# Kernel optimization log

Hardware: AMD Instinct MI355X
Metric: run time of the kernel (lower is better)

The kernel has to match this reference:

```python
import jax, jax.numpy as jnp
import numpy as np

GDEP = 3
ALPHA = 0.05
C_IN = 32
C_OUT = 32


def setup_inputs() -> dict:
    key = jax.random.key(0)
    k1, k2, k3, k4 = jax.random.split(key, 4)
    B, C, V, L = 16, C_IN, 512, 168
    x = jax.random.normal(k1, (B, C, V, L), dtype=jnp.float32)
    adj = jax.random.uniform(k2, (V, V), dtype=jnp.float32)
    fan_in = (GDEP + 1) * C_IN  # Conv2d 1x1: kaiming-uniform-ish init
    bound = 1.0 / np.sqrt(fan_in)
    W = jax.random.uniform(k3, (C_OUT, fan_in), minval=-bound, maxval=bound, dtype=jnp.float32)
    b = jax.random.uniform(k4, (C_OUT,), minval=-bound, maxval=bound, dtype=jnp.float32)
    return {"x": x, "adj": adj, "W": W, "b": b}


def reference(x, adj, W, b):
    V = adj.shape[0]
    a = adj + jnp.eye(V, dtype=adj.dtype)
    d = a.sum(axis=1)
    a = a / d[:, None]                      # row-normalized adjacency [V, V]
    h = x
    outs = [h]
    for _ in range(GDEP):                   # small fixed depth loop
        prop = jnp.einsum('ncvl,vw->ncwl', h, a)
        h = ALPHA * x + (1.0 - ALPHA) * prop
        outs.append(h)
    ho = jnp.concatenate(outs, axis=1)      # [B, (gdep+1)*C, V, L]
    # 1x1 conv == channel contraction
    out = jnp.einsum('bcvl,oc->bovl', ho, W) + b[None, :, None, None]
    return out
```

## Files before the change

kernel.cpp:

```cpp
#include <hip/hip_runtime.h>

#define V 512
#define L 168
#define PLANE 86016
#define CHSTRIDE 2752512
#define B_ 16
#define HDRE 1052672

typedef __attribute__((ext_vector_type(8))) short s16x8;
typedef __attribute__((ext_vector_type(4))) float f32x4;
typedef unsigned short u16;

__device__ inline short f2bf(float f) {
    unsigned u = __builtin_bit_cast(unsigned, f);
    u += 0x7FFF + ((u >> 16) & 1);
    return (short)(u >> 16);
}
__device__ inline float bf2f(u16 s) {
    return __builtin_bit_cast(float, ((unsigned)s) << 16);
}
__device__ inline void gll16(const u16* g, u16* lds) {
    __builtin_amdgcn_global_load_lds(
        (const __attribute__((address_space(1))) void*)g,
        (__attribute__((address_space(3))) void*)lds, 16, 0, 0);
}

__global__ __launch_bounds__(256) void prep2(const float* __restrict__ adj,
                                             const float* __restrict__ W,
                                             u16* __restrict__ M1,
                                             u16* __restrict__ ANb,
                                             u16* __restrict__ Wb) {
    if (blockIdx.x == V) {
        const float al = 0.05f, be = 0.95f;
        for (int i = threadIdx.x; i < 1024; i += 256) {
            const int o = i >> 5, c = i & 31;
            const float w0 = W[o * 128 + c];
            const float w1 = W[o * 128 + 32 + c];
            const float w2 = W[o * 128 + 64 + c];
            const float w3 = W[o * 128 + 96 + c];
            Wb[o * 128 + c]      = f2bf(w0 + al * (w1 + w2 + w3));
            Wb[o * 128 + 32 + c] = f2bf(be * (w1 + al * (w2 + w3)));
            Wb[o * 128 + 64 + c] = f2bf(be * be * (w2 + al * w3));
            Wb[o * 128 + 96 + c] = f2bf(be * be * be * w3);
        }
        return;
    }
    const int v = blockIdx.x;
    float s = 0.f;
    for (int w = threadIdx.x; w < V; w += 256)
        s += adj[v * V + w] + (w == v ? 1.f : 0.f);
    __shared__ float red[256];
    red[threadIdx.x] = s;
    __syncthreads();
    for (int off = 128; off > 0; off >>= 1) {
        if ((int)threadIdx.x < off) red[threadIdx.x] += red[threadIdx.x + off];
        __syncthreads();
    }
    const float inv = 1.f / red[0];
    for (int w = threadIdx.x; w < V; w += 256) {
        const short q = f2bf((adj[v * V + w] + (w == v ? 1.f : 0.f)) * inv);
        M1[w * V + v] = q;
        ANb[v * V + w] = q;
    }
}

__global__ __launch_bounds__(256) void powk(const u16* __restrict__ X,
                                            const u16* __restrict__ ANb,
                                            u16* __restrict__ OUT) {
    const int w0 = (blockIdx.x >> 3) * 64, v0 = (blockIdx.x & 7) * 64;
    const int tid = threadIdx.x, lane = tid & 63, wave = tid >> 6;
    const int colb = lane & 15, kg = lane >> 4;
    f32x4 acc[4];
#pragma unroll
    for (int i = 0; i < 4; i++) acc[i] = (f32x4){0.f, 0.f, 0.f, 0.f};
#pragma unroll 4
    for (int kk = 0; kk < 16; kk++) {
        const int u = kk * 32 + kg * 8;
        const s16x8 bfr = *(const s16x8*)&ANb[(size_t)(v0 + wave * 16 + colb) * 512 + u];
#pragma unroll
        for (int mt = 0; mt < 4; mt++) {
            const s16x8 afr = *(const s16x8*)&X[(size_t)(w0 + mt * 16 + colb) * 512 + u];
            acc[mt] = __builtin_amdgcn_mfma_f32_16x16x32_bf16(afr, bfr, acc[mt], 0, 0, 0);
        }
    }
#pragma unroll
    for (int mt = 0; mt < 4; mt++)
#pragma unroll
        for (int r = 0; r < 4; r++)
            OUT[(size_t)(w0 + mt * 16 + kg * 4 + r) * 512 + v0 + wave * 16 + colb] =
                (u16)f2bf(acc[mt][r]);
}

__global__ __launch_bounds__(256) void cvtT(const float* __restrict__ x,
                                            u16* __restrict__ xa) {
    const int b = blockIdx.z >> 5, c = blockIdx.z & 31;
    const int v0 = blockIdx.y * 64, l0 = blockIdx.x * 64;
    const int tid = threadIdx.x;
    __shared__ float T[64][65];
    const float* xp = x + (size_t)b * CHSTRIDE + (size_t)c * PLANE;
    u16* xo = xa + (size_t)b * CHSTRIDE;
#pragma unroll
    for (int rep = 0; rep < 16; rep++) {
        const int idx = rep * 256 + tid;
        const int vv = idx >> 6, ll = idx & 63;
        if (l0 + ll < L) T[vv][ll] = xp[(size_t)(v0 + vv) * L + l0 + ll];
    }
    __syncthreads();
#pragma unroll
    for (int rep = 0; rep < 16; rep++) {
        const int idx = rep * 256 + tid;
        const int ll = idx >> 6, vv = idx & 63;
        if (l0 + ll < L)
            xo[(size_t)((l0 + ll) * 32 + c) * 512 + v0 + vv] = f2bf(T[vv][ll]);
    }
}

__global__ __launch_bounds__(256, 2) void propOut(const u16* __restrict__ xa,
                                                  const u16* __restrict__ AS,
                                                  const u16* __restrict__ Wb,
                                                  const float* __restrict__ bias,
                                                  u16* __restrict__ tmpb) {
    const int b = blockIdx.z;
    const int logical = (blockIdx.x & 7) * 21 + (blockIdx.x >> 3);
    const int ntile = logical >> 2, wq = logical & 3;
    const int n0 = ntile * 128, w0 = wq * 128, l0 = ntile * 4;
    const int tid = threadIdx.x, lane = tid & 63, wave = tid >> 6;
    const int wm = wave >> 1, wn = wave & 1;
    const int colb = lane & 15, kg = lane >> 4;
    __shared__ __align__(16) u16 SH[2][16384];
    u16* flat = &SH[0][0];
    const size_t sB = (size_t)b * CHSTRIDE;
    const u16* srcb = xa + sB;

    const u16* gsrc = (wave == 3) ? srcb + (size_t)n0 * 512
                                  : AS + (size_t)wave * 262144 + (size_t)w0 * 512;

    f32x4 acc1[4][4], acc2[4][4], acc3[4][4];
#pragma unroll
    for (int i = 0; i < 4; i++)
#pragma unroll
        for (int j = 0; j < 4; j++) {
            acc1[i][j] = (f32x4){0.f, 0.f, 0.f, 0.f};
            acc2[i][j] = acc1[i][j];
            acc3[i][j] = acc1[i][j];
        }

#define STAGE(T, BUF)                                                             \
    {                                                                             \
        const int v0s = (T) * 32;                                                 \
        _Pragma("unroll") for (int i = 0; i < 8; i++) {                           \
            const int oct = i >> 1, half = i & 1;                                 \
            const int row = half * 64 + lane;                                     \
            gll16(gsrc + (size_t)row * 512 + v0s + oct * 8,                       \
                  &SH[BUF][wave * 4096 + oct * 1024 + half * 512]);               \
        }                                                                         \
    }

#define MFMASTEP(BUF)                                                             \
    {                                                                             \
        s16x8 bfr[4];                                                             \
        _Pragma("unroll") for (int nt = 0; nt < 4; nt++)                          \
            bfr[nt] = *(const s16x8*)&SH[BUF][12288 + kg * 1024 +                 \
                                             (wn * 64 + nt * 16 + colb) * 8];     \
        _Pragma("unroll") for (int mt = 0; mt < 4; mt++) {                        \
            const int aoff = kg * 1024 + (wm * 64 + mt * 16 + colb) * 8;          \
            const s16x8 a1 = *(const s16x8*)&SH[BUF][aoff];                       \
            const s16x8 a2 = *(const s16x8*)&SH[BUF][4096 + aoff];                \
            const s16x8 a3 = *(const s16x8*)&SH[BUF][8192 + aoff];                \
            _Pragma("unroll") for (int nt = 0; nt < 4; nt++) {                    \
                acc1[mt][nt] = __builtin_amdgcn_mfma_f32_16x16x32_bf16(           \
                    a1, bfr[nt], acc1[mt][nt], 0, 0, 0);                          \
                acc2[mt][nt] = __builtin_amdgcn_mfma_f32_16x16x32_bf16(           \
                    a2, bfr[nt], acc2[mt][nt], 0, 0, 0);                          \
                acc3[mt][nt] = __builtin_amdgcn_mfma_f32_16x16x32_bf16(           \
                    a3, bfr[nt], acc3[mt][nt], 0, 0, 0);                          \
            }                                                                     \
        }                                                                         \
    }

    STAGE(0, 0);
    __syncthreads();
#pragma unroll
    for (int t = 0; t < 16; t++) {
        const int buf = t & 1;
        if (t < 15) STAGE(t + 1, buf ^ 1);
        __builtin_amdgcn_s_setprio(1);
        MFMASTEP(buf);
        __builtin_amdgcn_s_setprio(0);
        __syncthreads();
    }
#undef MFMASTEP
#undef STAGE

#define BOUNCE(ACC)                                                               \
    _Pragma("unroll") for (int mt = 0; mt < 4; mt++) {                            \
        const int wr = wm * 64 + mt * 16 + kg * 4;                                \
        _Pragma("unroll") for (int nt = 0; nt < 4; nt++) {                        \
            const int nn = wn * 64 + nt * 16 + colb;                              \
            _Pragma("unroll") for (int r = 0; r < 4; r++)                         \
                flat[(wr + r) * 136 + nn] = (u16)f2bf(ACC[mt][nt][r]);            \
        }                                                                         \
    }

#define OUTACC(KP)                                                                \
    _Pragma("unroll") for (int pf = 0; pf < 8; pf++) {                            \
        const s16x8 bfr = *(const s16x8*)&flat[(pf * 16 + colb) * 136 +           \
                                               wave * 32 + kg * 8];               \
        _Pragma("unroll") for (int mt = 0; mt < 2; mt++) {                        \
            const s16x8 afr = *(const s16x8*)&Wb[(mt * 16 + colb) * 128 +         \
                                                 (KP) * 32 + kg * 8];             \
            aco[mt][pf] = __builtin_amdgcn_mfma_f32_16x16x32_bf16(                \
                afr, bfr, aco[mt][pf], 0, 0, 0);                                  \
        }                                                                         \
    }

    BOUNCE(acc1);
    __syncthreads();

    f32x4 aco[2][8];
#pragma unroll
    for (int i = 0; i < 2; i++)
#pragma unroll
        for (int j = 0; j < 8; j++) aco[i][j] = (f32x4){0.f, 0.f, 0.f, 0.f};

#pragma unroll
    for (int pf = 0; pf < 8; pf++) {
        s16x8 bfr;
#pragma unroll
        for (int j = 0; j < 8; j++)
            bfr[j] = (short)srcb[(size_t)(n0 + wave * 32 + kg * 8 + j) * 512 +
                                 w0 + pf * 16 + colb];
#pragma unroll
        for (int mt = 0; mt < 2; mt++) {
            const s16x8 afr = *(const s16x8*)&Wb[(mt * 16 + colb) * 128 + kg * 8];
            aco[mt][pf] = __builtin_amdgcn_mfma_f32_16x16x32_bf16(afr, bfr, aco[mt][pf], 0, 0, 0);
        }
    }
    OUTACC(1);
    __syncthreads();
    BOUNCE(acc2);
    __syncthreads();
    OUTACC(2);
    __syncthreads();
    BOUNCE(acc3);
    __syncthreads();
    OUTACC(3);
#undef BOUNCE
#undef OUTACC

#pragma unroll
    for (int mt = 0; mt < 2; mt++)
#pragma unroll
        for (int pf = 0; pf < 8; pf++)
#pragma unroll
            for (int r = 0; r < 4; r++) {
                const int o = mt * 16 + kg * 4 + r;
                tmpb[sB + (size_t)o * PLANE + (size_t)(l0 + wave) * 512 +
                     w0 + pf * 16 + colb] = (u16)f2bf(bias[o] + aco[mt][pf][r]);
            }
}

__global__ __launch_bounds__(256) void transT_b(const u16* __restrict__ tmpb,
                                                float* __restrict__ out) {
    const int o = blockIdx.y, b = blockIdx.z;
    const int vt = blockIdx.x / 3, lt = blockIdx.x % 3;
    const int v0 = vt * 64, l0 = lt * 64;
    const int tid = threadIdx.x;
    __shared__ float T[64][65];
    const u16* tp = tmpb + (size_t)b * CHSTRIDE + (size_t)o * PLANE;
    float* op = out + (size_t)b * CHSTRIDE + (size_t)o * PLANE;
#pragma unroll
    for (int rep = 0; rep < 16; rep++) {
        const int idx = rep * 256 + tid;
        const int ll = idx >> 6, vv = idx & 63;
        if (l0 + ll < L) T[ll][vv] = bf2f(tp[(size_t)(l0 + ll) * 512 + v0 + vv]);
    }
    __syncthreads();
#pragma unroll
    for (int rep = 0; rep < 16; rep++) {
        const int idx = rep * 256 + tid;
        const int vv = idx >> 6, ll = idx & 63;
        if (l0 + ll < L) op[(size_t)(v0 + vv) * L + l0 + ll] = T[ll][vv];
    }
}

extern "C" void kernel_launch(void* const* d_in, const int* in_sizes, int n_in,
                              void* d_out, int out_size, void* d_ws, size_t ws_size,
                              hipStream_t stream) {
    const float* x = (const float*)d_in[0];
    const float* adj = (const float*)d_in[1];
    const float* W = (const float*)d_in[2];
    const float* bias = (const float*)d_in[3];
    float* out = (float*)d_out;

    u16* hdr = (u16*)((char*)d_out + (size_t)out_size * 4 - (size_t)HDRE * 2 - 256);
    u16* AS = hdr;
    u16* M1 = AS;
    u16* M2 = AS + 262144;
    u16* M3 = AS + 2 * 262144;
    u16* ANb = AS + 3 * 262144;
    u16* Wb = AS + 4 * 262144;
    u16* hbuf = (u16*)d_ws;

    prep2<<<V + 1, 256, 0, stream>>>(adj, W, M1, ANb, Wb);
    powk<<<64, 256, 0, stream>>>(M1, ANb, M2);
    powk<<<64, 256, 0, stream>>>(M2, ANb, M3);

    int nbc = (int)(ws_size / ((size_t)4 * CHSTRIDE));
    if (nbc < 1) nbc = 1;
    if (nbc > B_) nbc = B_;

    for (int b0 = 0; b0 < B_; b0 += nbc) {
        const int nb = (B_ - b0 < nbc) ? (B_ - b0) : nbc;
        const float* xb = x + (size_t)b0 * CHSTRIDE;
        float* outb = out + (size_t)b0 * CHSTRIDE;
        u16* xa = hbuf;
        u16* tmpb = hbuf + (size_t)nbc * CHSTRIDE;

        cvtT<<<dim3(3, 8, nb * 32), 256, 0, stream>>>(xb, xa);
        propOut<<<dim3(168, 1, nb), 256, 0, stream>>>(xa, AS, Wb, bias, tmpb);
        transT_b<<<dim3(24, 32, nb), 256, 0, stream>>>(tmpb, outb);
    }
}
```

Baseline: 500.6 us.

## Restructure propagation GEMM to stream powers sequentially with K-tile 64

```diff
diff --git a/kernel.cpp b/kernel.cpp
--- a/kernel.cpp
+++ b/kernel.cpp
@@ -132,9 +132,6 @@
     const size_t sB = (size_t)b * CHSTRIDE;
     const u16* srcb = xa + sB;
 
-    const u16* gsrc = (wave == 3) ? srcb + (size_t)n0 * 512
-                                  : AS + (size_t)wave * 262144 + (size_t)w0 * 512;
-
     f32x4 acc1[4][4], acc2[4][4], acc3[4][4];
 #pragma unroll
     for (int i = 0; i < 4; i++)
@@ -147,45 +144,48 @@
 
 #define STAGE(T, BUF)                                                             \
     {                                                                             \
-        const int v0s = (T) * 32;                                                 \
-        _Pragma("unroll") for (int i = 0; i < 8; i++) {                           \
-            const int oct = i >> 1, half = i & 1;                                 \
+        const u16* Ak = AS + (size_t)((T) >> 3) * 262144;                         \
+        const int v0s = ((T) & 7) * 64;                                           \
+        _Pragma("unroll") for (int i = 0; i < 4; i++) {                           \
+            const int cc = wave * 4 + i, oct = cc >> 1, half = cc & 1;            \
             const int row = half * 64 + lane;                                     \
-            gll16(gsrc + (size_t)row * 512 + v0s + oct * 8,                       \
-                  &SH[BUF][wave * 4096 + oct * 1024 + half * 512]);               \
+            gll16(&Ak[(size_t)(w0 + row) * 512 + v0s + oct * 8],                  \
+                  &SH[BUF][oct * 1024 + half * 512]);                             \
+            gll16(&srcb[(size_t)(n0 + row) * 512 + v0s + oct * 8],                \
+                  &SH[BUF][8192 + oct * 1024 + half * 512]);                      \
         }                                                                         \
     }
 
-#define MFMASTEP(BUF)                                                             \
-    {                                                                             \
-        s16x8 bfr[4];                                                             \
+#define MFMASTEP(BUF, ACC)                                                        \
+    _Pragma("unroll") for (int kk = 0; kk < 2; kk++) {                            \
+        const int cq = kk * 4 + kg;                                               \
+        s16x8 afr[4], bfr[4];                                                     \
+        _Pragma("unroll") for (int mt = 0; mt < 4; mt++)                          \
+            afr[mt] = *(const s16x8*)&SH[BUF][cq * 1024 +                         \
+                                             (wm * 64 + mt * 16 + colb) * 8];     \
         _Pragma("unroll") for (int nt = 0; nt < 4; nt++)                          \
-            bfr[nt] = *(const s16x8*)&SH[BUF][12288 + kg * 1024 +                 \
+            bfr[nt] = *(const s16x8*)&SH[BUF][8192 + cq * 1024 +                  \
                                              (wn * 64 + nt * 16 + colb) * 8];     \
-        _Pragma("unroll") for (int mt = 0; mt < 4; mt++) {                        \
-            const int aoff = kg * 1024 + (wm * 64 + mt * 16 + colb) * 8;          \
-            const s16x8 a1 = *(const s16x8*)&SH[BUF][aoff];                       \
-            const s16x8 a2 = *(const s16x8*)&SH[BUF][4096 + aoff];                \
-            const s16x8 a3 = *(const s16x8*)&SH[BUF][8192 + aoff];                \
-            _Pragma("unroll") for (int nt = 0; nt < 4; nt++) {                    \
-                acc1[mt][nt] = __builtin_amdgcn_mfma_f32_16x16x32_bf16(           \
-                    a1, bfr[nt], acc1[mt][nt], 0, 0, 0);                          \
-                acc2[mt][nt] = __builtin_amdgcn_mfma_f32_16x16x32_bf16(           \
-                    a2, bfr[nt], acc2[mt][nt], 0, 0, 0);                          \
-                acc3[mt][nt] = __builtin_amdgcn_mfma_f32_16x16x32_bf16(           \
-                    a3, bfr[nt], acc3[mt][nt], 0, 0, 0);                          \
-            }                                                                     \
-        }                                                                         \
+        _Pragma("unroll") for (int mt = 0; mt < 4; mt++)                          \
+            _Pragma("unroll") for (int nt = 0; nt < 4; nt++)                      \
+                ACC[mt][nt] = __builtin_amdgcn_mfma_f32_16x16x32_bf16(            \
+                    afr[mt], bfr[nt], ACC[mt][nt], 0, 0, 0);                      \
     }
 
     STAGE(0, 0);
     __syncthreads();
 #pragma unroll
-    for (int t = 0; t < 16; t++) {
+    for (int t = 0; t < 24; t++) {
         const int buf = t & 1;
-        if (t < 15) STAGE(t + 1, buf ^ 1);
+        if (t < 23) STAGE(t + 1, buf ^ 1);
         __builtin_amdgcn_s_setprio(1);
-        MFMASTEP(buf);
+        if (t < 8) {
+            MFMASTEP(buf, acc1);
+        } else if (t < 16) {
+            MFMASTEP(buf, acc2);
+        } else {
+            MFMASTEP(buf, acc3);
+        }
         __builtin_amdgcn_s_setprio(0);
         __syncthreads();
     }
@@ -293,22 +293,32 @@
     const float* bias = (const float*)d_in[3];
     float* out = (float*)d_out;
 
-    u16* hdr = (u16*)((char*)d_out + (size_t)out_size * 4 - (size_t)HDRE * 2 - 256);
+    const bool single = ws_size >= (size_t)4 * CHSTRIDE * B_;
+    u16* hdr;
+    u16* hbuf;
+    int nbc;
+    if (single) {
+        hdr = (u16*)((char*)d_out + (size_t)out_size * 4 - (size_t)HDRE * 2 - 256);
+        hbuf = (u16*)d_ws;
+        nbc = B_;
+    } else {
+        hdr = (u16*)d_ws;
+        hbuf = (u16*)((char*)d_ws + (size_t)HDRE * 2 + 256);
+        const size_t avail = ws_size - (size_t)HDRE * 2 - 256;
+        nbc = (int)(avail / ((size_t)4 * CHSTRIDE));
+        if (nbc < 1) nbc = 1;
+        if (nbc > B_) nbc = B_;
+    }
     u16* AS = hdr;
     u16* M1 = AS;
     u16* M2 = AS + 262144;
     u16* M3 = AS + 2 * 262144;
     u16* ANb = AS + 3 * 262144;
     u16* Wb = AS + 4 * 262144;
-    u16* hbuf = (u16*)d_ws;
 
     prep2<<<V + 1, 256, 0, stream>>>(adj, W, M1, ANb, Wb);
     powk<<<64, 256, 0, stream>>>(M1, ANb, M2);
     powk<<<64, 256, 0, stream>>>(M2, ANb, M3);
-
-    int nbc = (int)(ws_size / ((size_t)4 * CHSTRIDE));
-    if (nbc < 1) nbc = 1;
-    if (nbc > B_) nbc = B_;
 
     for (int b0 = 0; b0 < B_; b0 += nbc) {
         const int nb = (B_ - b0 < nbc) ? (B_ - b0) : nbc;
```

After: 503.6 us. No clear change (+0.6%).
